# Optimization experiments

Measured on AMD Instinct MI355X. Metric: run time of the kernel, lower is better.

Reference implementation:

```python
import jax, jax.numpy as jnp
import numpy as np

N = 50000      # nodes
DEG = 16       # fixed neighbors per node
F = 128        # feat_dim
E = N * DEG    # edges
EPS = 1e-12


def setup_inputs() -> dict:
    key = jax.random.key(0)
    k_x, k_col = jax.random.split(key)
    x = jax.random.normal(k_x, (N, F), dtype=jnp.float32)
    col_id = jax.random.randint(k_col, (E,), 0, N, dtype=jnp.int32)
    row_ptr = (jnp.arange(N + 1, dtype=jnp.int32) * DEG)          # CSR offsets, fixed degree
    row_id = jnp.repeat(jnp.arange(N, dtype=jnp.int32), DEG)      # COO row index per edge
    beta = jnp.ones((1,), dtype=jnp.float32)
    return {"x": x, "row_id": row_id, "row_ptr": row_ptr, "col_id": col_id, "beta": beta}


def reference(x, row_id, row_ptr, col_id, beta):
    # AGNN: alpha_ij = softmax_j( beta * cos(x_i, x_j) ), out_i = sum_j alpha_ij * x_j
    n = x.shape[0]
    xn = x * jax.lax.rsqrt(jnp.sum(x * x, axis=-1, keepdims=True) + EPS)   # row-normalized
    # per-edge cosine similarity scaled by beta
    e = beta[0] * jnp.sum(xn[row_id] * xn[col_id], axis=-1)                # [E]
    # segment softmax over each row's neighborhood
    m = jax.ops.segment_max(e, row_id, num_segments=n)                      # [N]
    ee = jnp.exp(e - m[row_id])
    s = jax.ops.segment_sum(ee, row_id, num_segments=n)                     # [N]
    alpha = ee / s[row_id]                                                  # [E]
    # attention-weighted aggregation of raw neighbor features
    out = jax.ops.segment_sum(alpha[:, None] * x[col_id], row_id, num_segments=n)  # [N, F]
    return out
```

## Files before the change

kernel.cpp:

```cpp
#include <hip/hip_runtime.h>
#include <math.h>
#include <stdint.h>

#define DEG 16
#define FDIM 128
#define EPSV 1e-12f

#if __has_builtin(__builtin_amdgcn_sdot4)
#define SDOT4(a, b, c) __builtin_amdgcn_sdot4((int)(a), (int)(b), (c), false)
#else
__device__ __forceinline__ int SDOT4(uint32_t a, uint32_t b, int c) {
    return c + (int)(int8_t)(a & 255u) * (int)(int8_t)(b & 255u)
             + (int)(int8_t)((a >> 8) & 255u) * (int)(int8_t)((b >> 8) & 255u)
             + (int)(int8_t)((a >> 16) & 255u) * (int)(int8_t)((b >> 16) & 255u)
             + (int)(int8_t)(a >> 24) * (int)(int8_t)(b >> 24);
}
#endif

__global__ void agnn_prep_i8(const float* __restrict__ x,
                             uint32_t* __restrict__ xq,
                             float2* __restrict__ prm, int n) {
    int row  = (blockIdx.x * blockDim.x + threadIdx.x) >> 6;
    int lane = threadIdx.x & 63;
    if (row >= n) return;
    const float2 v = *reinterpret_cast<const float2*>(x + (size_t)row * FDIM + lane * 2);
    float s2 = v.x * v.x + v.y * v.y;
    float am = fmaxf(fabsf(v.x), fabsf(v.y));
#pragma unroll
    for (int off = 32; off >= 1; off >>= 1) {
        s2 += __shfl_xor(s2, off);
        am = fmaxf(am, __shfl_xor(am, off));
    }
    const float rn  = rsqrtf(s2 + EPSV);
    const float amc = fmaxf(am, 1e-20f);
    const float is  = 127.f / amc;
    const float s   = amc * (1.f / 127.f);
    const int q0 = (int)rintf(v.x * is);
    const int q1 = (int)rintf(v.y * is);
    reinterpret_cast<uint16_t*>(xq)[(size_t)row * 64 + lane] =
        (uint16_t)((q0 & 0xff) | ((q1 & 0xff) << 8));
    if (lane == 0) prm[row] = make_float2(s, s * rn);
}

__global__ __launch_bounds__(256, 8)
void agnn_main_v8(const uint32_t* __restrict__ xq,
                  const int* __restrict__ col_id,
                  const float2* __restrict__ prm,
                  const float* __restrict__ beta,
                  float* __restrict__ out, int n) {
    int node = (blockIdx.x * blockDim.x + threadIdx.x) >> 6;
    int lane = threadIdx.x & 63;
    if (node >= n) return;
    const int g = lane >> 4;
    const int t = lane & 15;

    const int4  c4 = *reinterpret_cast<const int4*>(col_id + node * DEG + 4 * g);
    const uint2 xi = *reinterpret_cast<const uint2*>(xq + (size_t)node * 32 + t * 2);
    const uint2 r0 = *reinterpret_cast<const uint2*>(xq + (size_t)c4.x * 32 + t * 2);
    const uint2 r1 = *reinterpret_cast<const uint2*>(xq + (size_t)c4.y * 32 + t * 2);
    const uint2 r2 = *reinterpret_cast<const uint2*>(xq + (size_t)c4.z * 32 + t * 2);
    const uint2 r3 = *reinterpret_cast<const uint2*>(xq + (size_t)c4.w * 32 + t * 2);
    const float2 pi = prm[node];
    const float2 p0 = prm[c4.x];
    const float2 p1 = prm[c4.y];
    const float2 p2 = prm[c4.z];
    const float2 p3 = prm[c4.w];
    const float b = beta[0];

    int d0 = SDOT4(r0.x, xi.x, SDOT4(r0.y, xi.y, 0));
    int d1 = SDOT4(r1.x, xi.x, SDOT4(r1.y, xi.y, 0));
    int d2 = SDOT4(r2.x, xi.x, SDOT4(r2.y, xi.y, 0));
    int d3 = SDOT4(r3.x, xi.x, SDOT4(r3.y, xi.y, 0));

#pragma unroll
    for (int off = 1; off < 16; off <<= 1) {
        d0 += __shfl_xor(d0, off);
        d1 += __shfl_xor(d1, off);
        d2 += __shfl_xor(d2, off);
        d3 += __shfl_xor(d3, off);
    }

    const float bt = b * pi.y;
    float w0 = __expf(bt * p0.y * (float)d0);
    float w1 = __expf(bt * p1.y * (float)d1);
    float w2 = __expf(bt * p2.y * (float)d2);
    float w3 = __expf(bt * p3.y * (float)d3);

    float sum = (w0 + w1) + (w2 + w3);
    sum += __shfl_xor(sum, 16);
    sum += __shfl_xor(sum, 32);
    const float inv = 1.f / sum;
    w0 *= inv * p0.x;
    w1 *= inv * p1.x;
    w2 *= inv * p2.x;
    w3 *= inv * p3.x;

    float acc[8];
#pragma unroll
    for (int k = 0; k < 4; ++k) {
        const float f0 = (float)(int)(int8_t)((r0.x >> (8 * k)) & 255u);
        const float f1 = (float)(int)(int8_t)((r1.x >> (8 * k)) & 255u);
        const float f2 = (float)(int)(int8_t)((r2.x >> (8 * k)) & 255u);
        const float f3 = (float)(int)(int8_t)((r3.x >> (8 * k)) & 255u);
        acc[k] = fmaf(w3, f3, fmaf(w2, f2, fmaf(w1, f1, w0 * f0)));
    }
#pragma unroll
    for (int k = 0; k < 4; ++k) {
        const float f0 = (float)(int)(int8_t)((r0.y >> (8 * k)) & 255u);
        const float f1 = (float)(int)(int8_t)((r1.y >> (8 * k)) & 255u);
        const float f2 = (float)(int)(int8_t)((r2.y >> (8 * k)) & 255u);
        const float f3 = (float)(int)(int8_t)((r3.y >> (8 * k)) & 255u);
        acc[4 + k] = fmaf(w3, f3, fmaf(w2, f2, fmaf(w1, f1, w0 * f0)));
    }

#pragma unroll
    for (int k = 0; k < 8; ++k) acc[k] += __shfl_xor(acc[k], 16);
#pragma unroll
    for (int k = 0; k < 8; ++k) acc[k] += __shfl_xor(acc[k], 32);

    if (g == 0) {
        float4* op = reinterpret_cast<float4*>(out + (size_t)node * FDIM + t * 8);
        op[0] = make_float4(acc[0], acc[1], acc[2], acc[3]);
        op[1] = make_float4(acc[4], acc[5], acc[6], acc[7]);
    }
}

__global__ void agnn_rnorm_kernel(const float* __restrict__ x,
                                  float* __restrict__ rn, int n) {
    int wave = (blockIdx.x * blockDim.x + threadIdx.x) >> 6;
    int lane = threadIdx.x & 63;
    if (wave >= n) return;
    const float2 v = *reinterpret_cast<const float2*>(x + (size_t)wave * FDIM + lane * 2);
    float s = v.x * v.x + v.y * v.y;
#pragma unroll
    for (int off = 32; off >= 1; off >>= 1)
        s += __shfl_xor(s, off);
    if (lane == 0) rn[wave] = rsqrtf(s + EPSV);
}

__global__ void agnn_main_f32(const float* __restrict__ x,
                              const int* __restrict__ col_id,
                              const float* __restrict__ rn,
                              const float* __restrict__ beta,
                              float* __restrict__ out, int n) {
    int wave = (blockIdx.x * blockDim.x + threadIdx.x) >> 6;
    int lane = threadIdx.x & 63;
    if (wave >= n) return;
    const int node = wave;
    const float b   = beta[0];
    const float rni = rn[node];
    const float2 xi = *reinterpret_cast<const float2*>(x + (size_t)node * FDIM + lane * 2);
    int cidx = col_id[node * DEG + (lane & 15)];
    float2 xj[DEG];
    float  p[DEG];
    float  rnj[DEG];
#pragma unroll
    for (int k = 0; k < DEG; ++k) {
        int cj = __shfl(cidx, k);
        const float2 v = *reinterpret_cast<const float2*>(x + (size_t)cj * FDIM + lane * 2);
        xj[k] = v; rnj[k] = rn[cj];
        p[k] = fmaf(xi.x, v.x, xi.y * v.y);
    }
#pragma unroll
    for (int off = 32; off >= 1; off >>= 1) {
#pragma unroll
        for (int k = 0; k < DEG; ++k)
            p[k] += __shfl_xor(p[k], off);
    }
    const float brni = b * rni;
#pragma unroll
    for (int k = 0; k < DEG; ++k) p[k] *= brni * rnj[k];
    float m = p[0];
#pragma unroll
    for (int k = 1; k < DEG; ++k) m = fmaxf(m, p[k]);
    float s = 0.f;
#pragma unroll
    for (int k = 0; k < DEG; ++k) { p[k] = __expf(p[k] - m); s += p[k]; }
    const float inv = 1.0f / s;
    float2 acc = make_float2(0.f, 0.f);
#pragma unroll
    for (int k = 0; k < DEG; ++k) {
        const float a = p[k] * inv;
        acc.x = fmaf(a, xj[k].x, acc.x);
        acc.y = fmaf(a, xj[k].y, acc.y);
    }
    *reinterpret_cast<float2*>(out + (size_t)node * FDIM + lane * 2) = acc;
}

extern "C" void kernel_launch(void* const* d_in, const int* in_sizes, int n_in,
                              void* d_out, int out_size, void* d_ws, size_t ws_size,
                              hipStream_t stream) {
    const float* x      = (const float*)d_in[0];
    const int*   col_id = (const int*)d_in[3];
    const float* beta   = (const float*)d_in[4];
    float*       out    = (float*)d_out;

    const int n = in_sizes[0] / FDIM;

    const int block = 256;
    const int wavesPerBlock = block / 64;
    const int grid = (n + wavesPerBlock - 1) / wavesPerBlock;

    const size_t xq_bytes = (size_t)n * FDIM;
    const size_t need = xq_bytes + (size_t)n * sizeof(float2);

    if (ws_size >= need) {
        uint32_t* xq  = (uint32_t*)d_ws;
        float2*   prm = (float2*)((char*)d_ws + xq_bytes);
        agnn_prep_i8<<<grid, block, 0, stream>>>(x, xq, prm, n);
        agnn_main_v8<<<grid, block, 0, stream>>>(xq, col_id, prm, beta, out, n);
    } else {
        float* rn = (float*)d_ws;
        agnn_rnorm_kernel<<<grid, block, 0, stream>>>(x, rn, n);
        agnn_main_f32<<<grid, block, 0, stream>>>(x, col_id, rn, beta, out, n);
    }
}
```

Baseline: 36.99 us.

## Use grid-stride persistent waves and nontemporal loads/stores in AGNN int8 kernel

The main kernel becomes a grid-stride loop over nodes with a fixed grid of 2048 blocks, so each wave handles several nodes instead of launching one wave per node. Streaming accesses (x in prep, col_id, and the output) now use nontemporal loads and stores so they do not displace the gathered int8 feature rows in cache. Output writes are split between two lane groups, each storing one float4, instead of one group writing both. The fixed grid trades block launch overhead for possible load imbalance and less latency hiding from oversubscription. The prep kernel now loads each float separately rather than as a float2.

```diff
diff --git a/kernel.cpp b/kernel.cpp
--- a/kernel.cpp
+++ b/kernel.cpp
@@ -5,6 +5,9 @@
 #define DEG 16
 #define FDIM 128
 #define EPSV 1e-12f
+
+typedef int   iv4 __attribute__((ext_vector_type(4)));
+typedef float fv4 __attribute__((ext_vector_type(4)));
 
 #if __has_builtin(__builtin_amdgcn_sdot4)
 #define SDOT4(a, b, c) __builtin_amdgcn_sdot4((int)(a), (int)(b), (c), false)
@@ -23,9 +26,10 @@
     int row  = (blockIdx.x * blockDim.x + threadIdx.x) >> 6;
     int lane = threadIdx.x & 63;
     if (row >= n) return;
-    const float2 v = *reinterpret_cast<const float2*>(x + (size_t)row * FDIM + lane * 2);
-    float s2 = v.x * v.x + v.y * v.y;
-    float am = fmaxf(fabsf(v.x), fabsf(v.y));
+    const float vx = __builtin_nontemporal_load(x + (size_t)row * FDIM + lane * 2);
+    const float vy = __builtin_nontemporal_load(x + (size_t)row * FDIM + lane * 2 + 1);
+    float s2 = vx * vx + vy * vy;
+    float am = fmaxf(fabsf(vx), fabsf(vy));
 #pragma unroll
     for (int off = 32; off >= 1; off >>= 1) {
         s2 += __shfl_xor(s2, off);
@@ -35,93 +39,100 @@
     const float amc = fmaxf(am, 1e-20f);
     const float is  = 127.f / amc;
     const float s   = amc * (1.f / 127.f);
-    const int q0 = (int)rintf(v.x * is);
-    const int q1 = (int)rintf(v.y * is);
+    const int q0 = (int)rintf(vx * is);
+    const int q1 = (int)rintf(vy * is);
     reinterpret_cast<uint16_t*>(xq)[(size_t)row * 64 + lane] =
         (uint16_t)((q0 & 0xff) | ((q1 & 0xff) << 8));
     if (lane == 0) prm[row] = make_float2(s, s * rn);
 }
 
 __global__ __launch_bounds__(256, 8)
-void agnn_main_v8(const uint32_t* __restrict__ xq,
-                  const int* __restrict__ col_id,
-                  const float2* __restrict__ prm,
-                  const float* __restrict__ beta,
-                  float* __restrict__ out, int n) {
-    int node = (blockIdx.x * blockDim.x + threadIdx.x) >> 6;
-    int lane = threadIdx.x & 63;
-    if (node >= n) return;
+void agnn_main_v10(const uint32_t* __restrict__ xq,
+                   const int* __restrict__ col_id,
+                   const float2* __restrict__ prm,
+                   const float* __restrict__ beta,
+                   float* __restrict__ out, int n) {
+    const int lane = threadIdx.x & 63;
+    const int wid  = (int)((blockIdx.x * blockDim.x + threadIdx.x) >> 6);
+    const int nw   = (int)((gridDim.x * blockDim.x) >> 6);
     const int g = lane >> 4;
     const int t = lane & 15;
-
-    const int4  c4 = *reinterpret_cast<const int4*>(col_id + node * DEG + 4 * g);
-    const uint2 xi = *reinterpret_cast<const uint2*>(xq + (size_t)node * 32 + t * 2);
-    const uint2 r0 = *reinterpret_cast<const uint2*>(xq + (size_t)c4.x * 32 + t * 2);
-    const uint2 r1 = *reinterpret_cast<const uint2*>(xq + (size_t)c4.y * 32 + t * 2);
-    const uint2 r2 = *reinterpret_cast<const uint2*>(xq + (size_t)c4.z * 32 + t * 2);
-    const uint2 r3 = *reinterpret_cast<const uint2*>(xq + (size_t)c4.w * 32 + t * 2);
-    const float2 pi = prm[node];
-    const float2 p0 = prm[c4.x];
-    const float2 p1 = prm[c4.y];
-    const float2 p2 = prm[c4.z];
-    const float2 p3 = prm[c4.w];
     const float b = beta[0];
 
-    int d0 = SDOT4(r0.x, xi.x, SDOT4(r0.y, xi.y, 0));
-    int d1 = SDOT4(r1.x, xi.x, SDOT4(r1.y, xi.y, 0));
-    int d2 = SDOT4(r2.x, xi.x, SDOT4(r2.y, xi.y, 0));
-    int d3 = SDOT4(r3.x, xi.x, SDOT4(r3.y, xi.y, 0));
-
-#pragma unroll
-    for (int off = 1; off < 16; off <<= 1) {
-        d0 += __shfl_xor(d0, off);
-        d1 += __shfl_xor(d1, off);
-        d2 += __shfl_xor(d2, off);
-        d3 += __shfl_xor(d3, off);
-    }
-
-    const float bt = b * pi.y;
-    float w0 = __expf(bt * p0.y * (float)d0);
-    float w1 = __expf(bt * p1.y * (float)d1);
-    float w2 = __expf(bt * p2.y * (float)d2);
-    float w3 = __expf(bt * p3.y * (float)d3);
-
-    float sum = (w0 + w1) + (w2 + w3);
-    sum += __shfl_xor(sum, 16);
-    sum += __shfl_xor(sum, 32);
-    const float inv = 1.f / sum;
-    w0 *= inv * p0.x;
-    w1 *= inv * p1.x;
-    w2 *= inv * p2.x;
-    w3 *= inv * p3.x;
-
-    float acc[8];
-#pragma unroll
-    for (int k = 0; k < 4; ++k) {
-        const float f0 = (float)(int)(int8_t)((r0.x >> (8 * k)) & 255u);
-        const float f1 = (float)(int)(int8_t)((r1.x >> (8 * k)) & 255u);
-        const float f2 = (float)(int)(int8_t)((r2.x >> (8 * k)) & 255u);
-        const float f3 = (float)(int)(int8_t)((r3.x >> (8 * k)) & 255u);
-        acc[k] = fmaf(w3, f3, fmaf(w2, f2, fmaf(w1, f1, w0 * f0)));
-    }
-#pragma unroll
-    for (int k = 0; k < 4; ++k) {
-        const float f0 = (float)(int)(int8_t)((r0.y >> (8 * k)) & 255u);
-        const float f1 = (float)(int)(int8_t)((r1.y >> (8 * k)) & 255u);
-        const float f2 = (float)(int)(int8_t)((r2.y >> (8 * k)) & 255u);
-        const float f3 = (float)(int)(int8_t)((r3.y >> (8 * k)) & 255u);
-        acc[4 + k] = fmaf(w3, f3, fmaf(w2, f2, fmaf(w1, f1, w0 * f0)));
-    }
-
-#pragma unroll
-    for (int k = 0; k < 8; ++k) acc[k] += __shfl_xor(acc[k], 16);
-#pragma unroll
-    for (int k = 0; k < 8; ++k) acc[k] += __shfl_xor(acc[k], 32);
-
-    if (g == 0) {
-        float4* op = reinterpret_cast<float4*>(out + (size_t)node * FDIM + t * 8);
-        op[0] = make_float4(acc[0], acc[1], acc[2], acc[3]);
-        op[1] = make_float4(acc[4], acc[5], acc[6], acc[7]);
+    for (int i = wid; i < n; i += nw) {
+        const iv4 c4 = __builtin_nontemporal_load(
+            reinterpret_cast<const iv4*>(col_id + (size_t)i * DEG + 4 * g));
+        const uint2 xi = *reinterpret_cast<const uint2*>(xq + (size_t)i * 32 + t * 2);
+        const uint2 r0 = *reinterpret_cast<const uint2*>(xq + (size_t)c4.x * 32 + t * 2);
+        const uint2 r1 = *reinterpret_cast<const uint2*>(xq + (size_t)c4.y * 32 + t * 2);
+        const uint2 r2 = *reinterpret_cast<const uint2*>(xq + (size_t)c4.z * 32 + t * 2);
+        const uint2 r3 = *reinterpret_cast<const uint2*>(xq + (size_t)c4.w * 32 + t * 2);
+        const float2 pi = prm[i];
+        const float2 p0 = prm[c4.x];
+        const float2 p1 = prm[c4.y];
+        const float2 p2 = prm[c4.z];
+        const float2 p3 = prm[c4.w];
+
+        int d0 = SDOT4(r0.x, xi.x, SDOT4(r0.y, xi.y, 0));
+        int d1 = SDOT4(r1.x, xi.x, SDOT4(r1.y, xi.y, 0));
+        int d2 = SDOT4(r2.x, xi.x, SDOT4(r2.y, xi.y, 0));
+        int d3 = SDOT4(r3.x, xi.x, SDOT4(r3.y, xi.y, 0));
+
+#pragma unroll
+        for (int off = 1; off < 16; off <<= 1) {
+            d0 += __shfl_xor(d0, off);
+            d1 += __shfl_xor(d1, off);
+            d2 += __shfl_xor(d2, off);
+            d3 += __shfl_xor(d3, off);
+        }
+
+        const float bt = b * pi.y;
+        float w0 = __expf(bt * p0.y * (float)d0);
+        float w1 = __expf(bt * p1.y * (float)d1);
+        float w2 = __expf(bt * p2.y * (float)d2);
+        float w3 = __expf(bt * p3.y * (float)d3);
+
+        float sum = (w0 + w1) + (w2 + w3);
+        sum += __shfl_xor(sum, 16);
+        sum += __shfl_xor(sum, 32);
+        const float inv = 1.f / sum;
+        w0 *= inv * p0.x;
+        w1 *= inv * p1.x;
+        w2 *= inv * p2.x;
+        w3 *= inv * p3.x;
+
+        float acc[8];
+#pragma unroll
+        for (int k = 0; k < 4; ++k) {
+            const float f0 = (float)(int)(int8_t)((r0.x >> (8 * k)) & 255u);
+            const float f1 = (float)(int)(int8_t)((r1.x >> (8 * k)) & 255u);
+            const float f2 = (float)(int)(int8_t)((r2.x >> (8 * k)) & 255u);
+            const float f3 = (float)(int)(int8_t)((r3.x >> (8 * k)) & 255u);
+            acc[k] = fmaf(w3, f3, fmaf(w2, f2, fmaf(w1, f1, w0 * f0)));
+        }
+#pragma unroll
+        for (int k = 0; k < 4; ++k) {
+            const float f0 = (float)(int)(int8_t)((r0.y >> (8 * k)) & 255u);
+            const float f1 = (float)(int)(int8_t)((r1.y >> (8 * k)) & 255u);
+            const float f2 = (float)(int)(int8_t)((r2.y >> (8 * k)) & 255u);
+            const float f3 = (float)(int)(int8_t)((r3.y >> (8 * k)) & 255u);
+            acc[4 + k] = fmaf(w3, f3, fmaf(w2, f2, fmaf(w1, f1, w0 * f0)));
+        }
+
+#pragma unroll
+        for (int k = 0; k < 8; ++k) acc[k] += __shfl_xor(acc[k], 16);
+#pragma unroll
+        for (int k = 0; k < 8; ++k) acc[k] += __shfl_xor(acc[k], 32);
+
+        if (g == 0) {
+            fv4 v; v.x = acc[0]; v.y = acc[1]; v.z = acc[2]; v.w = acc[3];
+            __builtin_nontemporal_store(
+                v, reinterpret_cast<fv4*>(out + (size_t)i * FDIM + t * 8));
+        } else if (g == 1) {
+            fv4 v; v.x = acc[4]; v.y = acc[5]; v.z = acc[6]; v.w = acc[7];
+            __builtin_nontemporal_store(
+                v, reinterpret_cast<fv4*>(out + (size_t)i * FDIM + t * 8 + 4));
+        }
     }
 }
 
@@ -199,7 +210,7 @@
 
     const int block = 256;
     const int wavesPerBlock = block / 64;
-    const int grid = (n + wavesPerBlock - 1) / wavesPerBlock;
+    const int gridPrep = (n + wavesPerBlock - 1) / wavesPerBlock;
 
     const size_t xq_bytes = (size_t)n * FDIM;
     const size_t need = xq_bytes + (size_t)n * sizeof(float2);
@@ -207,11 +218,11 @@
     if (ws_size >= need) {
         uint32_t* xq  = (uint32_t*)d_ws;
         float2*   prm = (float2*)((char*)d_ws + xq_bytes);
-        agnn_prep_i8<<<grid, block, 0, stream>>>(x, xq, prm, n);
-        agnn_main_v8<<<grid, block, 0, stream>>>(xq, col_id, prm, beta, out, n);
+        agnn_prep_i8<<<gridPrep, block, 0, stream>>>(x, xq, prm, n);
+        agnn_main_v10<<<2048, block, 0, stream>>>(xq, col_id, prm, beta, out, n);
     } else {
         float* rn = (float*)d_ws;
-        agnn_rnorm_kernel<<<grid, block, 0, stream>>>(x, rn, n);
-        agnn_main_f32<<<grid, block, 0, stream>>>(x, col_id, rn, beta, out, n);
-    }
-}
+        agnn_rnorm_kernel<<<gridPrep, block, 0, stream>>>(x, rn, n);
+        agnn_main_f32<<<gridPrep, block, 0, stream>>>(x, col_id, rn, beta, out, n);
+    }
+}
```

Result: slower. 47.83 us (+29.3%).
